# Optimization experiments

Measured on AMD Instinct MI355X. Metric: run time of the kernel, lower is better.

Reference implementation:

```python
import jax, jax.numpy as jnp
import numpy as np
import math

B, S, D = 16, 2048, 128

def setup_inputs() -> dict:
    key = jax.random.key(0)
    k1, k2, k3, k4 = jax.random.split(key, 4)
    query = jax.random.normal(k1, (B, S, D), dtype=jnp.float32)
    key_t = jax.random.normal(k2, (B, S, D), dtype=jnp.float32)
    value = jax.random.normal(k3, (B, S, D), dtype=jnp.float32)
    attn_mask = jax.random.randint(k4, (B, S, S), 0, 2).astype(bool)
    return {"query": query, "key": key_t, "value": value, "attn_mask": attn_mask}

def reference(query, key, value, attn_mask):
    # score = Q K^T / sqrt(d)  -> [B, Sq, Sk]
    scale = 1.0 / math.sqrt(query.shape[-1])
    score = jnp.einsum('bqd,bkd->bqk', query, key) * scale
    # faithful quirk: masked positions are replaced by the VALUE 1e-9 (not -inf)
    mask_score = jnp.where(attn_mask, jnp.float32(1e-9), score)
    # faithful quirk: softmax over dim=1 (the query axis), as in the torch source
    score_matrix = jax.nn.softmax(mask_score, axis=1)
    # output = softmax(scores) @ V  -> [B, Sq, D]
    output = jnp.einsum('bqk,bkd->bqd', score_matrix, value)
    return output
```

## Files before the change

### kernel.cpp

```cpp
#include <hip/hip_runtime.h>
#include <math.h>

#define NB 16
#define SS 2048
#define DQ 128
#define SCALE 0.08838834764831845f

typedef __bf16 bf16x8 __attribute__((ext_vector_type(8)));
typedef unsigned short ushort8_t __attribute__((ext_vector_type(8)));
typedef float floatx4 __attribute__((ext_vector_type(4)));

__device__ __forceinline__ unsigned short f2bf(float x) {
  unsigned int u = __float_as_uint(x);
  u += 0x7fffu + ((u >> 16) & 1u);
  return (unsigned short)(u >> 16);
}
union FragU { ushort8_t u; bf16x8 b; };
__device__ __forceinline__ bf16x8 ld_frag(const unsigned short* p) {
  FragU t; t.u = *(const ushort8_t*)p; return t.b;
}
__device__ __forceinline__ floatx4 mfma16(bf16x8 a, bf16x8 b, floatx4 c) {
  return __builtin_amdgcn_mfma_f32_16x16x32_bf16(a, b, c, 0, 0, 0);
}

__device__ __forceinline__ void bar_lds() {
  asm volatile("s_waitcnt lgkmcnt(0)\n\ts_barrier" ::: "memory");
}


__global__ void zero_accum(float* __restrict__ O) {
  float* p = O + (size_t)blockIdx.x * SS * DQ + 16 * DQ;
#pragma unroll
  for (int i = 0; i < 8; ++i) p[threadIdx.x + 256 * i] = 0.f;
}

template<int WRITE_E>
__global__ __launch_bounds__(256, 3) void pass1_colsum(
    const float* __restrict__ Q, const float* __restrict__ K,
    const int* __restrict__ M, float* __restrict__ O,
    unsigned short* __restrict__ E)
{
  const int k0  = blockIdx.x * 128;
  const int b   = blockIdx.y;
  const int qc  = blockIdx.z;
  const int tid = threadIdx.x;
  const int w = tid >> 6, lane = tid & 63, l15 = lane & 15, quad = lane >> 4;

  __shared__ unsigned short Kbf[128][136];
  __shared__ unsigned short Qbf[64][136];

  const float* Qb = Q + (size_t)b * SS * DQ;
  const float* Kb = K + (size_t)b * SS * DQ;
  const int*   Mb = M + (size_t)b * SS * SS;
  unsigned short* Eb = WRITE_E ? (E + (size_t)b * SS * SS) : nullptr;

  const int srow = tid >> 5;
  const int sc4  = (tid & 31) * 4;

#pragma unroll
  for (int r = 0; r < 16; ++r) {
    int row = srow + r * 8;
    float4 v = *(const float4*)(Kb + (size_t)(k0 + row) * DQ + sc4);
    *(ushort4*)&Kbf[row][sc4] = make_ushort4(f2bf(v.x), f2bf(v.y), f2bf(v.z), f2bf(v.w));
  }

  const int qlane = 16 * w + l15;

  float4 qreg[8];
  int4 mv_nxt[8];
  {
    const int q0 = qc * 512;
#pragma unroll
    for (int r = 0; r < 8; ++r)
      qreg[r] = *(const float4*)(Qb + (size_t)(q0 + srow + r * 8) * DQ + sc4);
#pragma unroll
    for (int t2 = 0; t2 < 2; ++t2)
#pragma unroll
      for (int i = 0; i < 4; ++i)
        mv_nxt[t2 * 4 + i] = *(const int4*)(Mb + (size_t)(q0 + qlane) * SS +
                                            k0 + t2 * 64 + 16 * i + quad * 4);
  }

  float colacc[32];
#pragma unroll
  for (int t = 0; t < 32; ++t) colacc[t] = 0.f;

  for (int qi = 0; qi < 8; ++qi) {
    bar_lds();
    int4 mv[8];
#pragma unroll
    for (int t = 0; t < 8; ++t) mv[t] = mv_nxt[t];
#pragma unroll
    for (int r = 0; r < 8; ++r) {
      float4 v = qreg[r];
      *(ushort4*)&Qbf[srow + r * 8][sc4] =
          make_ushort4(f2bf(v.x), f2bf(v.y), f2bf(v.z), f2bf(v.w));
    }
    bar_lds();
    if (qi < 7) {
      const int qn = qc * 512 + (qi + 1) * 64;
#pragma unroll
      for (int r = 0; r < 8; ++r)
        qreg[r] = *(const float4*)(Qb + (size_t)(qn + srow + r * 8) * DQ + sc4);
#pragma unroll
      for (int t2 = 0; t2 < 2; ++t2)
#pragma unroll
        for (int i = 0; i < 4; ++i)
          mv_nxt[t2 * 4 + i] = *(const int4*)(Mb + (size_t)(qn + qlane) * SS +
                                              k0 + t2 * 64 + 16 * i + quad * 4);
    }

    floatx4 acc[8];
#pragma unroll
    for (int i = 0; i < 8; ++i) acc[i] = (floatx4){0.f, 0.f, 0.f, 0.f};
#pragma unroll
    for (int d0 = 0; d0 < DQ; d0 += 32) {
      bf16x8 bq = ld_frag(&Qbf[qlane][d0 + quad * 8]);
#pragma unroll
      for (int i = 0; i < 4; ++i) {
        bf16x8 ak0 = ld_frag(&Kbf[16 * i + l15][d0 + quad * 8]);
        acc[i] = mfma16(ak0, bq, acc[i]);
        bf16x8 ak1 = ld_frag(&Kbf[64 + 16 * i + l15][d0 + quad * 8]);
        acc[4 + i] = mfma16(ak1, bq, acc[4 + i]);
      }
    }
    const int qrow = qc * 512 + qi * 64 + qlane;
#pragma unroll
    for (int t2 = 0; t2 < 2; ++t2) {
#pragma unroll
      for (int i = 0; i < 4; ++i) {
        int4 mvw = mv[t2 * 4 + i];
        int mm[4] = {mvw.x, mvw.y, mvw.z, mvw.w};
        float ev[4];
#pragma unroll
        for (int r = 0; r < 4; ++r) {
          float s = mm[r] ? 1e-9f : acc[t2 * 4 + i][r] * SCALE;
          ev[r] = __expf(s);
          colacc[t2 * 16 + i * 4 + r] += ev[r];
        }
        if (WRITE_E) {
          *(ushort4*)(Eb + (size_t)qrow * SS + k0 + t2 * 64 + 16 * i + quad * 4) =
              make_ushort4(f2bf(ev[0]), f2bf(ev[1]), f2bf(ev[2]), f2bf(ev[3]));
        }
      }
    }
  }

#pragma unroll
  for (int t = 0; t < 32; ++t) {
    colacc[t] += __shfl_xor(colacc[t], 1, 64);
    colacc[t] += __shfl_xor(colacc[t], 2, 64);
    colacc[t] += __shfl_xor(colacc[t], 4, 64);
    colacc[t] += __shfl_xor(colacc[t], 8, 64);
  }
  bar_lds();
  float* red = (float*)&Qbf[0][0];
  if (l15 == 0) {
#pragma unroll
    for (int t2 = 0; t2 < 2; ++t2)
#pragma unroll
      for (int i = 0; i < 4; ++i)
#pragma unroll
        for (int r = 0; r < 4; ++r)
          red[w * 128 + t2 * 64 + 16 * i + quad * 4 + r] =
              colacc[t2 * 16 + i * 4 + r];
  }
  bar_lds();
  if (tid < 128) {
    float s = red[tid] + red[128 + tid] + red[256 + tid] + red[384 + tid];
    atomicAdd(O + (size_t)b * SS * DQ + 16 * DQ + k0 + tid, s);
  }
}

__global__ void combine_linv(float* __restrict__ O) {
  const int b  = blockIdx.x;
  const int jb = blockIdx.y * 4;
  float* Ob = O + (size_t)b * SS * DQ;
#pragma unroll
  for (int it = 0; it < 8; ++it) {
    int k = threadIdx.x + 256 * it;
    float inv = 1.0f / Ob[16 * DQ + k];
#pragma unroll
    for (int j = 0; j < 4; ++j)
      Ob[(size_t)(64 * (jb + j)) * DQ + k] = inv;
  }
}

__global__ __launch_bounds__(256, 2) void pass2_pv(
    const float* __restrict__ V, const unsigned short* __restrict__ E,
    float* __restrict__ O)
{
  const int b = blockIdx.y, q0 = blockIdx.x * 64;
  const int tid = threadIdx.x;
  const int w = tid >> 6, lane = tid & 63, l15 = lane & 15, quad = lane >> 4;

  __shared__ unsigned short Wt[128][72];
  __shared__ float Li[SS];

  const float* Vb = V + (size_t)b * SS * DQ;
  const unsigned short* Erow =
      E + (size_t)b * SS * SS + (size_t)(q0 + 16 * w + l15) * SS;

  const int sc4 = (tid & 31) * 4;
  const int vk2 = (tid >> 5) * 2;

  {
    const float* src = O + ((size_t)b * SS + q0) * DQ;
#pragma unroll
    for (int r = 0; r < 2; ++r) {
      int idx = (tid + r * 256) * 4;
      *(float4*)&Li[idx] = *(const float4*)(src + idx);
    }
  }

  floatx4 accO[8];
#pragma unroll
  for (int j = 0; j < 8; ++j) accO[j] = (floatx4){0.f, 0.f, 0.f, 0.f};

  float4 vreg[8];
  FragU ef_nxt[2];
  {
#pragma unroll
    for (int r = 0; r < 4; ++r) {
      int k2 = vk2 + r * 16;
      vreg[2 * r]     = *(const float4*)(Vb + (size_t)(k2)     * DQ + sc4);
      vreg[2 * r + 1] = *(const float4*)(Vb + (size_t)(k2 + 1) * DQ + sc4);
    }
#pragma unroll
    for (int c = 0; c < 2; ++c)
      ef_nxt[c].u = *(const ushort8_t*)(Erow + 32 * c + quad * 8);
  }

  for (int k0 = 0; k0 < SS; k0 += 64) {
    bar_lds();
    FragU ef[2] = {ef_nxt[0], ef_nxt[1]};

#pragma unroll
    for (int r = 0; r < 4; ++r) {
      int k2 = vk2 + r * 16;
      float la = Li[k0 + k2], lb = Li[k0 + k2 + 1];
      float fa[4] = {vreg[2*r].x * la, vreg[2*r].y * la,
                     vreg[2*r].z * la, vreg[2*r].w * la};
      float fb[4] = {vreg[2*r+1].x * lb, vreg[2*r+1].y * lb,
                     vreg[2*r+1].z * lb, vreg[2*r+1].w * lb};
#pragma unroll
      for (int i = 0; i < 4; ++i) {
        int d  = sc4 + i;
        int kk = k2 ^ ((((unsigned)d >> 2) & 7) << 3);
        *(ushort2*)&Wt[d][kk] = make_ushort2(f2bf(fa[i]), f2bf(fb[i]));
      }
    }
    bar_lds();

    if (k0 + 64 < SS) {
      const int kn = k0 + 64;
#pragma unroll
      for (int r = 0; r < 4; ++r) {
        int k2 = vk2 + r * 16;
        vreg[2 * r]     = *(const float4*)(Vb + (size_t)(kn + k2)     * DQ + sc4);
        vreg[2 * r + 1] = *(const float4*)(Vb + (size_t)(kn + k2 + 1) * DQ + sc4);
      }
#pragma unroll
      for (int c = 0; c < 2; ++c)
        ef_nxt[c].u = *(const ushort8_t*)(Erow + kn + 32 * c + quad * 8);
    }

#pragma unroll
    for (int c = 0; c < 2; ++c) {
      bf16x8 be = ef[c].b;
#pragma unroll
      for (int j = 0; j < 8; ++j) {
        int d  = 16 * j + l15;
        int kk = (32 * c + quad * 8) ^ ((((unsigned)d >> 2) & 7) << 3);
        bf16x8 aw = ld_frag(&Wt[d][kk]);
        accO[j] = mfma16(aw, be, accO[j]);
      }
    }
  }

#pragma unroll
  for (int j = 0; j < 8; ++j) {
    float* op = O + ((size_t)b * SS + q0 + 16 * w + l15) * DQ + 16 * j + quad * 4;
    *(float4*)op = make_float4(accO[j][0], accO[j][1], accO[j][2], accO[j][3]);
  }
}

__global__ __launch_bounds__(256, 2) void pass2_out(
    const float* __restrict__ Q, const float* __restrict__ K,
    const float* __restrict__ V, const int* __restrict__ M,
    float* __restrict__ O)
{
  const int b = blockIdx.y, q0 = blockIdx.x * 64;
  const int tid = threadIdx.x;
  const int w = tid >> 6, lane = tid & 63, l15 = lane & 15, quad = lane >> 4;

  __shared__ unsigned short Kbf[64][136];
  __shared__ unsigned short Es[64][72];
  __shared__ unsigned short Wt[128][72];
  __shared__ float Li[SS];

  const float* Qb = Q + (size_t)b * SS * DQ;
  const float* Kb = K + (size_t)b * SS * DQ;
  const float* Vb = V + (size_t)b * SS * DQ;
  const int*   Mb = M + (size_t)b * SS * SS;

  const int srow = tid >> 5;
  const int sc4  = (tid & 31) * 4;

  {
    const float* src = O + ((size_t)b * SS + q0) * DQ;
#pragma unroll
    for (int r = 0; r < 2; ++r) {
      int idx = (tid + r * 256) * 4;
      *(float4*)&Li[idx] = *(const float4*)(src + idx);
    }
  }
  FragU qf[4];
  {
    const float* qrow = Qb + (size_t)(q0 + 16 * w + l15) * DQ;
#pragma unroll
    for (int i = 0; i < 4; ++i) {
      float4 a = *(const float4*)(qrow + 32 * i + quad * 8);
      float4 c = *(const float4*)(qrow + 32 * i + quad * 8 + 4);
      qf[i].u = (ushort8_t){f2bf(a.x), f2bf(a.y), f2bf(a.z), f2bf(a.w),
                            f2bf(c.x), f2bf(c.y), f2bf(c.z), f2bf(c.w)};
    }
  }

  floatx4 accO[8];
#pragma unroll
  for (int j = 0; j < 8; ++j) accO[j] = (floatx4){0.f, 0.f, 0.f, 0.f};

  const int* mrow = Mb + (size_t)(q0 + 16 * w + l15) * SS;

  float4 kreg[8], vreg[8];
  int4 mv_nxt[4];
  const int vk2 = (tid >> 5) * 2;
  {
#pragma unroll
    for (int r = 0; r < 8; ++r)
      kreg[r] = *(const float4*)(Kb + (size_t)(srow + r * 8) * DQ + sc4);
#pragma unroll
    for (int r = 0; r < 4; ++r) {
      int k2 = vk2 + r * 16;
      vreg[2 * r]     = *(const float4*)(Vb + (size_t)(k2)     * DQ + sc4);
      vreg[2 * r + 1] = *(const float4*)(Vb + (size_t)(k2 + 1) * DQ + sc4);
    }
#pragma unroll
    for (int j = 0; j < 4; ++j)
      mv_nxt[j] = *(const int4*)(mrow + 16 * j + quad * 4);
  }

  for (int k0 = 0; k0 < SS; k0 += 64) {
    bar_lds();
    int4 mv[4] = {mv_nxt[0], mv_nxt[1], mv_nxt[2], mv_nxt[3]};

#pragma unroll
    for (int r = 0; r < 8; ++r) {
      float4 v = kreg[r];
      *(ushort4*)&Kbf[srow + r * 8][sc4] =
          make_ushort4(f2bf(v.x), f2bf(v.y), f2bf(v.z), f2bf(v.w));
    }
#pragma unroll
    for (int r = 0; r < 4; ++r) {
      int k2 = vk2 + r * 16;
      float fa[4] = {vreg[2*r].x, vreg[2*r].y, vreg[2*r].z, vreg[2*r].w};
      float fb[4] = {vreg[2*r+1].x, vreg[2*r+1].y, vreg[2*r+1].z, vreg[2*r+1].w};
#pragma unroll
      for (int i = 0; i < 4; ++i) {
        int d  = sc4 + i;
        int kk = k2 ^ ((((unsigned)d >> 2) & 7) << 3);
        *(ushort2*)&Wt[d][kk] = make_ushort2(f2bf(fa[i]), f2bf(fb[i]));
      }
    }
    bar_lds();

    if (k0 + 64 < SS) {
      const int kn = k0 + 64;
#pragma unroll
      for (int r = 0; r < 8; ++r)
        kreg[r] = *(const float4*)(Kb + (size_t)(kn + srow + r * 8) * DQ + sc4);
#pragma unroll
      for (int r = 0; r < 4; ++r) {
        int k2 = vk2 + r * 16;
        vreg[2 * r]     = *(const float4*)(Vb + (size_t)(kn + k2)     * DQ + sc4);
        vreg[2 * r + 1] = *(const float4*)(Vb + (size_t)(kn + k2 + 1) * DQ + sc4);
      }
#pragma unroll
      for (int j = 0; j < 4; ++j)
        mv_nxt[j] = *(const int4*)(mrow + kn + 16 * j + quad * 4);
    }

    floatx4 acc[4];
#pragma unroll
    for (int j = 0; j < 4; ++j) acc[j] = (floatx4){0.f, 0.f, 0.f, 0.f};
#pragma unroll
    for (int i = 0; i < 4; ++i) {
      bf16x8 bq = qf[i].b;
#pragma unroll
      for (int j = 0; j < 4; ++j) {
        bf16x8 ak = ld_frag(&Kbf[16 * j + l15][32 * i + quad * 8]);
        acc[j] = mfma16(ak, bq, acc[j]);
      }
    }
#pragma unroll
    for (int j = 0; j < 4; ++j) {
      float4 liv = *(const float4*)&Li[k0 + 16 * j + quad * 4];
      float lv[4] = {liv.x, liv.y, liv.z, liv.w};
      int mm[4] = {mv[j].x, mv[j].y, mv[j].z, mv[j].w};
      unsigned short es[4];
#pragma unroll
      for (int r = 0; r < 4; ++r) {
        float s = mm[r] ? 1e-9f : acc[j][r] * SCALE;
        es[r] = f2bf(__expf(s) * lv[r]);
      }
      *(ushort4*)&Es[16 * w + l15][16 * j + quad * 4] =
          make_ushort4(es[0], es[1], es[2], es[3]);
    }
#pragma unroll
    for (int c = 0; c < 2; ++c) {
      bf16x8 be = ld_frag(&Es[16 * w + l15][32 * c + quad * 8]);
#pragma unroll
      for (int j = 0; j < 8; ++j) {
        int d  = 16 * j + l15;
        int kk = (32 * c + quad * 8) ^ ((((unsigned)d >> 2) & 7) << 3);
        bf16x8 aw = ld_frag(&Wt[d][kk]);
        accO[j] = mfma16(aw, be, accO[j]);
      }
    }
  }

#pragma unroll
  for (int j = 0; j < 8; ++j) {
    float* op = O + ((size_t)b * SS + q0 + 16 * w + l15) * DQ + 16 * j + quad * 4;
    *(float4*)op = make_float4(accO[j][0], accO[j][1], accO[j][2], accO[j][3]);
  }
}

extern "C" void kernel_launch(void* const* d_in, const int* in_sizes, int n_in,
                              void* d_out, int out_size, void* d_ws, size_t ws_size,
                              hipStream_t stream) {
  const float* Q = (const float*)d_in[0];
  const float* K = (const float*)d_in[1];
  const float* V = (const float*)d_in[2];
  const int*   M = (const int*)d_in[3];
  float* O = (float*)d_out;

  const size_t eneed = (size_t)NB * SS * SS * sizeof(unsigned short);

  zero_accum<<<dim3(NB), 256, 0, stream>>>(O);
  if (d_ws != nullptr && ws_size >= eneed) {
    unsigned short* E = (unsigned short*)d_ws;
    pass1_colsum<1><<<dim3(16, NB, 4), 256, 0, stream>>>(Q, K, M, O, E);
    combine_linv<<<dim3(NB, 8), 256, 0, stream>>>(O);
    pass2_pv<<<dim3(32, NB), 256, 0, stream>>>(V, E, O);
  } else {
    pass1_colsum<0><<<dim3(16, NB, 4), 256, 0, stream>>>(Q, K, M, O, nullptr);
    combine_linv<<<dim3(NB, 8), 256, 0, stream>>>(O);
    pass2_out<<<dim3(32, NB), 256, 0, stream>>>(Q, K, V, M, O);
  }
}
```

Baseline: 506.7 us.

## Double-buffer the scaled-V LDS tile in pass2_pv to drop one barrier per step

The PV pass now keeps two LDS copies of the transposed, Li-scaled bf16 V tile. Each iteration runs MFMAs on the current buffer while building the next buffer and prefetching V and E two steps ahead, so only one barrier is needed per iteration instead of two. LDS use per block roughly doubles for the Wt tile, which could limit occupancy, and register pressure rises from the deeper prefetch.

```diff
diff --git a/kernel.cpp b/kernel.cpp
--- a/kernel.cpp
+++ b/kernel.cpp
@@ -194,7 +194,7 @@
   const int tid = threadIdx.x;
   const int w = tid >> 6, lane = tid & 63, l15 = lane & 15, quad = lane >> 4;
 
-  __shared__ unsigned short Wt[128][72];
+  __shared__ unsigned short Wt[2][128][72];
   __shared__ float Li[SS];
 
   const float* Vb = V + (size_t)b * SS * DQ;
@@ -218,62 +218,87 @@
   for (int j = 0; j < 8; ++j) accO[j] = (floatx4){0.f, 0.f, 0.f, 0.f};
 
   float4 vreg[8];
-  FragU ef_nxt[2];
-  {
-#pragma unroll
-    for (int r = 0; r < 4; ++r) {
-      int k2 = vk2 + r * 16;
-      vreg[2 * r]     = *(const float4*)(Vb + (size_t)(k2)     * DQ + sc4);
-      vreg[2 * r + 1] = *(const float4*)(Vb + (size_t)(k2 + 1) * DQ + sc4);
-    }
-#pragma unroll
-    for (int c = 0; c < 2; ++c)
-      ef_nxt[c].u = *(const ushort8_t*)(Erow + 32 * c + quad * 8);
-  }
-
-  for (int k0 = 0; k0 < SS; k0 += 64) {
+  FragU ef_cur[2], ef_nxt[2];
+#pragma unroll
+  for (int r = 0; r < 4; ++r) {
+    int k2 = vk2 + r * 16;
+    vreg[2 * r]     = *(const float4*)(Vb + (size_t)(k2)     * DQ + sc4);
+    vreg[2 * r + 1] = *(const float4*)(Vb + (size_t)(k2 + 1) * DQ + sc4);
+  }
+  ef_cur[0].u = *(const ushort8_t*)(Erow + quad * 8);
+  ef_cur[1].u = *(const ushort8_t*)(Erow + 32 + quad * 8);
+
+  bar_lds();
+
+#pragma unroll
+  for (int r = 0; r < 4; ++r) {
+    int k2 = vk2 + r * 16;
+    float la = Li[k2], lb = Li[k2 + 1];
+    float fa[4] = {vreg[2*r].x * la, vreg[2*r].y * la,
+                   vreg[2*r].z * la, vreg[2*r].w * la};
+    float fb[4] = {vreg[2*r+1].x * lb, vreg[2*r+1].y * lb,
+                   vreg[2*r+1].z * lb, vreg[2*r+1].w * lb};
+#pragma unroll
+    for (int i = 0; i < 4; ++i) {
+      int d  = sc4 + i;
+      int kk = k2 ^ ((((unsigned)d >> 2) & 7) << 3);
+      *(ushort2*)&Wt[0][d][kk] = make_ushort2(f2bf(fa[i]), f2bf(fb[i]));
+    }
+  }
+#pragma unroll
+  for (int r = 0; r < 4; ++r) {
+    int k2 = vk2 + r * 16;
+    vreg[2 * r]     = *(const float4*)(Vb + (size_t)(64 + k2)     * DQ + sc4);
+    vreg[2 * r + 1] = *(const float4*)(Vb + (size_t)(64 + k2 + 1) * DQ + sc4);
+  }
+  ef_nxt[0].u = *(const ushort8_t*)(Erow + 64 + quad * 8);
+  ef_nxt[1].u = *(const ushort8_t*)(Erow + 96 + quad * 8);
+
+  for (int it = 0; it < 32; ++it) {
+    const int cur = it & 1;
     bar_lds();
-    FragU ef[2] = {ef_nxt[0], ef_nxt[1]};
-
-#pragma unroll
-    for (int r = 0; r < 4; ++r) {
-      int k2 = vk2 + r * 16;
-      float la = Li[k0 + k2], lb = Li[k0 + k2 + 1];
-      float fa[4] = {vreg[2*r].x * la, vreg[2*r].y * la,
-                     vreg[2*r].z * la, vreg[2*r].w * la};
-      float fb[4] = {vreg[2*r+1].x * lb, vreg[2*r+1].y * lb,
-                     vreg[2*r+1].z * lb, vreg[2*r+1].w * lb};
-#pragma unroll
-      for (int i = 0; i < 4; ++i) {
-        int d  = sc4 + i;
-        int kk = k2 ^ ((((unsigned)d >> 2) & 7) << 3);
-        *(ushort2*)&Wt[d][kk] = make_ushort2(f2bf(fa[i]), f2bf(fb[i]));
-      }
-    }
-    bar_lds();
-
-    if (k0 + 64 < SS) {
-      const int kn = k0 + 64;
-#pragma unroll
-      for (int r = 0; r < 4; ++r) {
-        int k2 = vk2 + r * 16;
-        vreg[2 * r]     = *(const float4*)(Vb + (size_t)(kn + k2)     * DQ + sc4);
-        vreg[2 * r + 1] = *(const float4*)(Vb + (size_t)(kn + k2 + 1) * DQ + sc4);
-      }
-#pragma unroll
-      for (int c = 0; c < 2; ++c)
-        ef_nxt[c].u = *(const ushort8_t*)(Erow + kn + 32 * c + quad * 8);
-    }
 
 #pragma unroll
     for (int c = 0; c < 2; ++c) {
-      bf16x8 be = ef[c].b;
+      bf16x8 be = ef_cur[c].b;
 #pragma unroll
       for (int j = 0; j < 8; ++j) {
         int d  = 16 * j + l15;
         int kk = (32 * c + quad * 8) ^ ((((unsigned)d >> 2) & 7) << 3);
-        bf16x8 aw = ld_frag(&Wt[d][kk]);
+        bf16x8 aw = ld_frag(&Wt[cur][d][kk]);
         accO[j] = mfma16(aw, be, accO[j]);
+      }
+    }
+
+    if (it < 31) {
+      const int kn = (it + 1) * 64;
+#pragma unroll
+      for (int r = 0; r < 4; ++r) {
+        int k2 = vk2 + r * 16;
+        float la = Li[kn + k2], lb = Li[kn + k2 + 1];
+        float fa[4] = {vreg[2*r].x * la, vreg[2*r].y * la,
+                       vreg[2*r].z * la, vreg[2*r].w * la};
+        float fb[4] = {vreg[2*r+1].x * lb, vreg[2*r+1].y * lb,
+                       vreg[2*r+1].z * lb, vreg[2*r+1].w * lb};
+#pragma unroll
+        for (int i = 0; i < 4; ++i) {
+          int d  = sc4 + i;
+          int kk = k2 ^ ((((unsigned)d >> 2) & 7) << 3);
+          *(ushort2*)&Wt[cur ^ 1][d][kk] = make_ushort2(f2bf(fa[i]), f2bf(fb[i]));
+        }
+      }
+      ef_cur[0] = ef_nxt[0];
+      ef_cur[1] = ef_nxt[1];
+      if (it < 30) {
+        const int kp = (it + 2) * 64;
+#pragma unroll
+        for (int r = 0; r < 4; ++r) {
+          int k2 = vk2 + r * 16;
+          vreg[2 * r]     = *(const float4*)(Vb + (size_t)(kp + k2)     * DQ + sc4);
+          vreg[2 * r + 1] = *(const float4*)(Vb + (size_t)(kp + k2 + 1) * DQ + sc4);
+        }
+        ef_nxt[0].u = *(const ushort8_t*)(Erow + kp + quad * 8);
+        ef_nxt[1].u = *(const ushort8_t*)(Erow + kp + 32 + quad * 8);
       }
     }
   }
```

Measured after the change: 512.3 us. No clear change (+1.1%).
